# Optimization experiments

Measured on AMD Instinct MI355X. Metric: run time of the kernel, lower is better.

Reference implementation:

```python
import jax, jax.numpy as jnp
import numpy as np

EPS = 1e-5
NUM_GROUPS = 8

def group_norm(x, gamma, beta):
    B, C, D, H, W = x.shape
    g = NUM_GROUPS
    xg = x.reshape(B, g, C // g, D, H, W)
    mu = xg.mean(axis=(2, 3, 4, 5), keepdims=True)
    var = xg.var(axis=(2, 3, 4, 5), keepdims=True)
    xn = ((xg - mu) / jnp.sqrt(var + EPS)).reshape(B, C, D, H, W)
    return xn * gamma[None, :, None, None, None] + beta[None, :, None, None, None]

def setup_inputs() -> dict:
    key = jax.random.key(0)
    ks = jax.random.split(key, 7)
    B, C, D, H, W = 4, 256, 16, 16, 16
    x = jax.random.normal(ks[0], (B, C, D, H, W), dtype=jnp.float32)
    gn_gamma = jnp.ones((C,), dtype=jnp.float32)
    gn_beta = jnp.zeros((C,), dtype=jnp.float32)
    # 1x1x1 conv weights stored as [out, in] matrices
    s = 1.0 / np.sqrt(C)
    qkv_w = jax.random.uniform(ks[1], (3 * C, C), minval=-s, maxval=s, dtype=jnp.float32)
    qkv_b = jax.random.uniform(ks[2], (3 * C,), minval=-s, maxval=s, dtype=jnp.float32)
    proj_w = jax.random.uniform(ks[3], (C, C), minval=-s, maxval=s, dtype=jnp.float32)
    proj_b = jax.random.uniform(ks[4], (C,), minval=-s, maxval=s, dtype=jnp.float32)
    return {"x": x, "gn_gamma": gn_gamma, "gn_beta": gn_beta,
            "qkv_w": qkv_w, "qkv_b": qkv_b, "proj_w": proj_w, "proj_b": proj_b}

def reference(x, gn_gamma, gn_beta, qkv_w, qkv_b, proj_w, proj_b):
    B, C, D, H, W = x.shape
    N = D * H * W
    h = group_norm(x, gn_gamma, gn_beta)
    hf = h.reshape(B, C, N)  # (B, C, N)
    # 1x1x1 conv == channel matmul
    qkv = jnp.einsum('oc,bcn->bon', qkv_w, hf) + qkv_b[None, :, None]  # (B, 3C, N)
    q, k, v = jnp.split(qkv, 3, axis=1)  # each (B, C, N)
    q = q.transpose(0, 2, 1)  # (B, N, C)
    k = k.transpose(0, 2, 1)
    v = v.transpose(0, 2, 1)
    scale = C ** (-0.5)
    attn = jnp.einsum('bnc,bmc->bnm', q, k) * scale  # (B, N, N)
    attn = jax.nn.softmax(attn, axis=-1)
    o = jnp.einsum('bnm,bmc->bnc', attn, v)  # (B, N, C)
    o = o.transpose(0, 2, 1)  # (B, C, N)
    o = jnp.einsum('oc,bcn->bon', proj_w, o) + proj_b[None, :, None]
    return x + o.reshape(B, C, D, H, W)
```

## Files before the change

kernel.cpp:

```cpp
#include <hip/hip_runtime.h>
#include <hip/hip_bf16.h>

typedef unsigned short u16;
typedef unsigned int u32;
typedef __attribute__((ext_vector_type(8))) short short8;
typedef __attribute__((ext_vector_type(4))) short short4v;
typedef __attribute__((ext_vector_type(4))) float f32x4;

static __device__ __forceinline__ u16 f2bf(float f) {
    union { float f; unsigned u; } a; a.f = f;
    unsigned u = a.u;
    u += 0x7FFFu + ((u >> 16) & 1u);
    return (u16)(u >> 16);
}
static __device__ __forceinline__ float bf2f(u16 h) {
    union { u32 u; float f; } a; a.u = ((u32)h) << 16; return a.f;
}
static __device__ __forceinline__ u32 cvtpk(float lo, float hi) {
    u32 r; asm("v_cvt_pk_bf16_f32 %0, %1, %2" : "=v"(r) : "v"(lo), "v"(hi)); return r;
}
static __device__ __forceinline__ void gload16(const u16* g, u16* l) {
    __builtin_amdgcn_global_load_lds((const __attribute__((address_space(1))) u32*)(const void*)g,
                                     (__attribute__((address_space(3))) u32*)(void*)l, 16, 0, 0);
}

__global__ __launch_bounds__(256) void k_pre(const float* __restrict__ x, float* __restrict__ pstats,
                                             const float* __restrict__ qw, const float* __restrict__ pw,
                                             u16* __restrict__ q2, u16* __restrict__ p2) {
    const int t = threadIdx.x;
    if (blockIdx.x >= 256) {
        const int i = ((int)blockIdx.x - 256) * 1024 + t * 4;
        const float* src; u16* dst;
        if (i < 196608) { src = qw + i; dst = q2 + i; }
        else            { src = pw + (i - 196608); dst = p2 + (i - 196608); }
        float4 v = *reinterpret_cast<const float4*>(src);
        u16 o[4] = { f2bf(v.x), f2bf(v.y), f2bf(v.z), f2bf(v.w) };
        *reinterpret_cast<uint2*>(dst) = *reinterpret_cast<uint2*>(o);
        return;
    }
    const int bg = blockIdx.x >> 3, sl = blockIdx.x & 7;
    const float* p = x + (size_t)bg * 131072 + sl * 16384;
    float s = 0.f, ss = 0.f;
#pragma unroll
    for (int i = t * 4; i < 16384; i += 256 * 4) {
        float4 v = *reinterpret_cast<const float4*>(p + i);
        s  += v.x + v.y + v.z + v.w;
        ss += v.x * v.x + v.y * v.y + v.z * v.z + v.w * v.w;
    }
    for (int off = 1; off < 64; off <<= 1) { s += __shfl_xor(s, off); ss += __shfl_xor(ss, off); }
    __shared__ float ls[4], lss[4];
    if ((t & 63) == 0) { ls[t >> 6] = s; lss[t >> 6] = ss; }
    __syncthreads();
    if (t == 0) {
        pstats[(bg * 8 + sl) * 2]     = ls[0] + ls[1] + ls[2] + ls[3];
        pstats[(bg * 8 + sl) * 2 + 1] = lss[0] + lss[1] + lss[2] + lss[3];
    }
}

__global__ __launch_bounds__(256) void k_norm(const float* __restrict__ x, const float* __restrict__ gamma,
                                              const float* __restrict__ beta, const float* __restrict__ pstats,
                                              u16* __restrict__ H) {
    __shared__ u16 T[64][72];
    __shared__ float smu[2], srs[2];
    const int b = blockIdx.z, c0 = blockIdx.y * 64, n0 = blockIdx.x * 64;
    const int t = threadIdx.x;
    if (t < 2) {
        const int g = (c0 >> 5) + t;
        float S = 0.f, SS = 0.f;
#pragma unroll
        for (int sl = 0; sl < 8; ++sl) {
            S  += pstats[((b * 8 + g) * 8 + sl) * 2];
            SS += pstats[((b * 8 + g) * 8 + sl) * 2 + 1];
        }
        const float inv = 1.f / (32.f * 4096.f);
        float mu  = S * inv;
        float var = SS * inv - mu * mu;
        smu[t] = mu;
        srs[t] = rsqrtf(var + 1e-5f);
    }
    __syncthreads();
    const int cl = t >> 2, nb = (t & 3) * 16;
    const int c = c0 + cl;
    const float mu = smu[cl >> 5];
    const float rstd = srs[cl >> 5];
    const float ga = gamma[c] * rstd, be = beta[c] - mu * ga;
    const float* xp = &x[((size_t)b * 256 + c) * 4096 + n0 + nb];
#pragma unroll
    for (int j = 0; j < 16; j += 4) {
        float4 v = *reinterpret_cast<const float4*>(xp + j);
        T[cl][nb + j + 0] = f2bf(v.x * ga + be);
        T[cl][nb + j + 1] = f2bf(v.y * ga + be);
        T[cl][nb + j + 2] = f2bf(v.z * ga + be);
        T[cl][nb + j + 3] = f2bf(v.w * ga + be);
    }
    __syncthreads();
    const int nl = t >> 2, cb = (t & 3) * 16;
    short8 s0, s1;
#pragma unroll
    for (int j = 0; j < 8; ++j) { s0[j] = (short)T[cb + j][nl]; s1[j] = (short)T[cb + 8 + j][nl]; }
    u16* dst = &H[((size_t)b * 4096 + n0 + nl) * 256 + c0 + cb];
    *reinterpret_cast<short8*>(dst)     = s0;
    *reinterpret_cast<short8*>(dst + 8) = s1;
}

__global__ __launch_bounds__(256) void k_qkv(const u16* __restrict__ H, const u16* __restrict__ W2,
                                             const float* __restrict__ qkv_b,
                                             u16* __restrict__ Q, u16* __restrict__ K, u16* __restrict__ V) {
    __shared__ u16 T[9216];
    const int b = blockIdx.z, o0 = blockIdx.x * 64, nb0 = blockIdx.y * 128;
    const int t = threadIdx.x, w = t >> 6, l = t & 63, lr = l & 15, lg = l >> 4;
    const size_t bN = (size_t)b * 4096;
    f32x4 acc[2][4];
#pragma unroll
    for (int m = 0; m < 2; ++m)
#pragma unroll
        for (int nf = 0; nf < 4; ++nf) acc[m][nf] = f32x4{0.f, 0.f, 0.f, 0.f};
    const u16* A0 = &H[(bN + nb0 + w * 32 + lr) * 256];
    const u16* A1 = A0 + 16 * 256;
#pragma unroll
    for (int cc = 0; cc < 8; ++cc) {
        short8 af0 = *reinterpret_cast<const short8*>(A0 + cc * 32 + lg * 8);
        short8 af1 = *reinterpret_cast<const short8*>(A1 + cc * 32 + lg * 8);
#pragma unroll
        for (int nf = 0; nf < 4; ++nf) {
            short8 bf = *reinterpret_cast<const short8*>(&W2[(size_t)(o0 + nf * 16 + lr) * 256 + cc * 32 + lg * 8]);
            acc[0][nf] = __builtin_amdgcn_mfma_f32_16x16x32_bf16(af0, bf, acc[0][nf], 0, 0, 0);
            acc[1][nf] = __builtin_amdgcn_mfma_f32_16x16x32_bf16(af1, bf, acc[1][nf], 0, 0, 0);
        }
    }
    const int og = o0 >> 8;
    const float scal = (og == 0) ? 0.0625f * 1.44269504f : 1.0f;
    float bias[4];
#pragma unroll
    for (int nf = 0; nf < 4; ++nf) bias[nf] = qkv_b[o0 + nf * 16 + lr];
    if (og < 2) {
#pragma unroll
        for (int m = 0; m < 2; ++m)
#pragma unroll
            for (int nf = 0; nf < 4; ++nf)
#pragma unroll
                for (int i = 0; i < 4; ++i)
                    T[(w * 32 + m * 16 + lg * 4 + i) * 72 + nf * 16 + lr] = f2bf((acc[m][nf][i] + bias[nf]) * scal);
        __syncthreads();
        const int rl = t >> 1, half = (t & 1) * 32;
        u16* dst = (og == 0 ? Q : K) + (bN + nb0 + rl) * 256 + (o0 & 255) + half;
#pragma unroll
        for (int j = 0; j < 4; ++j)
            *reinterpret_cast<short8*>(dst + j * 8) = *reinterpret_cast<short8*>(&T[rl * 72 + half + j * 8]);
    } else {
#pragma unroll
        for (int m = 0; m < 2; ++m)
#pragma unroll
            for (int nf = 0; nf < 4; ++nf)
#pragma unroll
                for (int i = 0; i < 4; ++i)
                    T[(nf * 16 + lr) * 144 + w * 32 + m * 16 + lg * 4 + i] = f2bf(acc[m][nf][i] + bias[nf]);
        __syncthreads();
        const int ol = t >> 2, nbl = (t & 3) * 32;
        const int s_ = (ol >> 1) & 7;
        u16* dst = V + ((size_t)b * 256 + (o0 - 512) + ol) * 4096 + nb0 + nbl;
#pragma unroll
        for (int j = 0; j < 4; ++j) {
            short8 vv = *reinterpret_cast<short8*>(&T[ol * 144 + nbl + j * 8]);
            short8 ov;
            if (s_ & 1) ov = short8{vv[4], vv[5], vv[6], vv[7], vv[0], vv[1], vv[2], vv[3]};
            else        ov = vv;
            *reinterpret_cast<short8*>(dst + (((2 * j) ^ (s_ & 6)) * 4)) = ov;
        }
    }
}

__global__ __launch_bounds__(512, 1) void k_flash(const u16* __restrict__ Qw, const u16* __restrict__ Kw,
                                                  const u16* __restrict__ Vw, u16* __restrict__ Opart,
                                                  float* __restrict__ ml) {
    __shared__ u16 Ks[2][16384];
    __shared__ u16 Vs[2][16384];
    const int sp = blockIdx.x, b = blockIdx.y;
    const int tid = threadIdx.x;
    const int w = tid >> 6, l = tid & 63;
    const int lr = l & 15, lg = l >> 4;
    const int qbase = blockIdx.z * 256 + w * 32;
    const int kb0 = sp * 1024;
    const size_t bN = (size_t)b * 4096;

    const u16* srcK = Kw + (bN + kb0 + (tid >> 5)) * 256 + (((tid & 31) * 8) ^ (((tid >> 5) & 7) * 8));
    const int u = tid & 255, sth = tid >> 8;
    const u16* srcV = Vw + ((size_t)b * 256 + (u >> 2)) * 4096 + kb0 + sth * 32 + (u & 3) * 8;
    const int vdst = sth * 8192 + u * 8;

#define STAGE(d, toff) { \
        const u16* sk_ = srcK + (size_t)(toff) * 16384; \
        const u16* sv_ = srcV + (toff) * 64; \
        gload16(sk_,               Ks[d] + tid * 8); \
        gload16(sk_ + 16 * 256,    Ks[d] + 4096 + tid * 8); \
        gload16(sk_ + 32 * 256,    Ks[d] + 8192 + tid * 8); \
        gload16(sk_ + 48 * 256,    Ks[d] + 12288 + tid * 8); \
        gload16(sv_,               Vs[d] + vdst); \
        gload16(sv_ + 64 * 4096,   Vs[d] + vdst + 2048); \
        gload16(sv_ + 128 * 4096,  Vs[d] + vdst + 4096); \
        gload16(sv_ + 192 * 4096,  Vs[d] + vdst + 6144); }

    const int c6 = (lr >> 2) & 1;
    int kofs[2];
#pragma unroll
    for (int n = 0; n < 2; ++n) kofs[n] = (n * 16 + lr) * 256 + ((lg * 8) ^ ((lr & 3) * 8));
    const int vslotA = ((lg ^ (lr >> 1)) * 4);
    const int vslotB = vslotA ^ 16;

    short8 qf[2][8];
#pragma unroll
    for (int m = 0; m < 2; ++m)
#pragma unroll
        for (int cc = 0; cc < 8; ++cc)
            qf[m][cc] = *reinterpret_cast<const short8*>(&Qw[(bN + qbase + m * 16 + lr) * 256 + cc * 32 + lg * 8]);

    f32x4 Oa[2][16];
    float mr[2], lsum[2];
#pragma unroll
    for (int m = 0; m < 2; ++m) {
#pragma unroll
        for (int cs = 0; cs < 16; ++cs) Oa[m][cs] = f32x4{0.f, 0.f, 0.f, 0.f};
        mr[m] = -1e30f; lsum[m] = 0.f;
    }

#define QK_PHASE(scv, ST) { \
        const int kO_ = (ST) * 8192; \
        _Pragma("unroll") \
        for (int m = 0; m < 2; ++m) \
            _Pragma("unroll") \
            for (int n = 0; n < 2; ++n) scv[m][n] = f32x4{0.f, 0.f, 0.f, 0.f}; \
        __builtin_amdgcn_s_setprio(1); \
        _Pragma("unroll") \
        for (int cc = 0; cc < 8; ++cc) { \
            const int cb_ = ((cc ^ c6) << 5); \
            short8 kf0 = *reinterpret_cast<const short8*>(&Ks[d][kO_ + kofs[0] + cb_]); \
            short8 kf1 = *reinterpret_cast<const short8*>(&Ks[d][kO_ + kofs[1] + cb_]); \
            scv[0][0] = __builtin_amdgcn_mfma_f32_16x16x32_bf16(kf0, qf[0][cc], scv[0][0], 0, 0, 0); \
            scv[0][1] = __builtin_amdgcn_mfma_f32_16x16x32_bf16(kf1, qf[0][cc], scv[0][1], 0, 0, 0); \
            scv[1][0] = __builtin_amdgcn_mfma_f32_16x16x32_bf16(kf0, qf[1][cc], scv[1][0], 0, 0, 0); \
            scv[1][1] = __builtin_amdgcn_mfma_f32_16x16x32_bf16(kf1, qf[1][cc], scv[1][1], 0, 0, 0); \
        } \
        __builtin_amdgcn_s_setprio(0); }

#define SM_PHASE(scv, pfv) { \
        float tmax_[2]; \
        bool need_ = false; \
        _Pragma("unroll") \
        for (int m = 0; m < 2; ++m) { \
            float tm = fmaxf(fmaxf(fmaxf(scv[m][0][0], scv[m][0][1]), fmaxf(scv[m][0][2], scv[m][0][3])), \
                             fmaxf(fmaxf(scv[m][1][0], scv[m][1][1]), fmaxf(scv[m][1][2], scv[m][1][3]))); \
            tm = fmaxf(tm, __shfl_xor(tm, 16)); \
            tm = fmaxf(tm, __shfl_xor(tm, 32)); \
            tmax_[m] = tm; \
            need_ = need_ || (tm > mr[m] + 8.f); \
        } \
        if (__any(need_)) { \
            float av_[2][4]; \
            _Pragma("unroll") \
            for (int m = 0; m < 2; ++m) { \
                float mn = fmaxf(mr[m], tmax_[m]); \
                float al = exp2f(mr[m] - mn); \
                mr[m] = mn; \
                lsum[m] *= al; \
                _Pragma("unroll") \
                for (int i = 0; i < 4; ++i) av_[m][i] = __shfl(al, lg * 4 + i); \
            } \
            _Pragma("unroll") \
            for (int m = 0; m < 2; ++m) \
                _Pragma("unroll") \
                for (int cs = 0; cs < 16; ++cs) \
                    _Pragma("unroll") \
                    for (int i = 0; i < 4; ++i) Oa[m][cs][i] *= av_[m][i]; \
        } \
        _Pragma("unroll") \
        for (int m = 0; m < 2; ++m) { \
            float p_[8]; \
            float la_ = 0.f; \
            _Pragma("unroll") \
            for (int n = 0; n < 2; ++n) \
                _Pragma("unroll") \
                for (int i = 0; i < 4; ++i) { \
                    float pv = exp2f(scv[m][n][i] - mr[m]); \
                    la_ += pv; \
                    p_[n * 4 + i] = pv; \
                } \
            lsum[m] += la_; \
            _Pragma("unroll") \
            for (int j = 0; j < 4; ++j) pfv[m][j] = cvtpk(p_[2 * j], p_[2 * j + 1]); \
        } }

#define PV_PHASE(pfv, ST) { \
        const int vH_ = (ST) * 8192; \
        union { u32 uw[4]; short8 v; } pa_, pb_; \
        _Pragma("unroll") \
        for (int j = 0; j < 4; ++j) { pa_.uw[j] = pfv[0][j]; pb_.uw[j] = pfv[1][j]; } \
        __builtin_amdgcn_s_setprio(1); \
        _Pragma("unroll") \
        for (int cs = 0; cs < 16; ++cs) { \
            const int base_ = vH_ + (cs * 16 + lr) * 32; \
            short4v lo = *reinterpret_cast<const short4v*>(&Vs[d][base_ + vslotA]); \
            short4v hi = *reinterpret_cast<const short4v*>(&Vs[d][base_ + vslotB]); \
            short8 vf = __builtin_shufflevector(lo, hi, 0, 1, 2, 3, 4, 5, 6, 7); \
            Oa[0][cs] = __builtin_amdgcn_mfma_f32_16x16x32_bf16(pa_.v, vf, Oa[0][cs], 0, 0, 0); \
            Oa[1][cs] = __builtin_amdgcn_mfma_f32_16x16x32_bf16(pb_.v, vf, Oa[1][cs], 0, 0, 0); \
        } \
        __builtin_amdgcn_s_setprio(0); }

    STAGE(0, 0);
    for (int kt = 0; kt < 16; ++kt) {
        const int d = kt & 1;
        asm volatile("s_waitcnt vmcnt(0)" ::: "memory");
        __builtin_amdgcn_sched_barrier(0);
        __builtin_amdgcn_s_barrier();
        if (kt < 15) STAGE(d ^ 1, kt + 1);

        f32x4 sc[2][2];
        u32 pf0[2][4], pf1[2][4];
        QK_PHASE(sc, 0);
        SM_PHASE(sc, pf0);
        QK_PHASE(sc, 1);
        PV_PHASE(pf0, 0);
        SM_PHASE(sc, pf1);
        PV_PHASE(pf1, 1);
    }
#undef STAGE
#undef QK_PHASE
#undef SM_PHASE
#undef PV_PHASE

    float lt[2];
#pragma unroll
    for (int m = 0; m < 2; ++m) {
        float ts = lsum[m];
        ts += __shfl_xor(ts, 16);
        ts += __shfl_xor(ts, 32);
        lt[m] = ts;
    }
    const size_t obase = ((size_t)(b * 4 + sp) * 4096 + qbase);
#pragma unroll
    for (int m = 0; m < 2; ++m)
#pragma unroll
        for (int cs = 0; cs < 16; ++cs)
#pragma unroll
            for (int i = 0; i < 4; ++i)
                Opart[(obase + m * 16 + lg * 4 + i) * 256 + cs * 16 + lr] = f2bf(Oa[m][cs][i]);
    if (lg == 0) {
#pragma unroll
        for (int m = 0; m < 2; ++m) {
            size_t r = obase + m * 16 + lr;
            ml[r * 2]     = mr[m];
            ml[r * 2 + 1] = lt[m];
        }
    }
}

__global__ __launch_bounds__(256) void k_comb(const u16* __restrict__ Opart, const float* __restrict__ ml,
                                              u16* __restrict__ Obf) {
    const int row = blockIdx.x * 8 + (threadIdx.x >> 5);
    const int b = row >> 12;
    const int c0 = (threadIdx.x & 31) * 8;
    const size_t rbase = (size_t)b * 4 * 4096 + (row & 4095);
    float ms[4], lsv[4];
#pragma unroll
    for (int s = 0; s < 4; ++s) {
        ms[s]  = ml[(rbase + (size_t)s * 4096) * 2];
        lsv[s] = ml[(rbase + (size_t)s * 4096) * 2 + 1];
    }
    float M = fmaxf(fmaxf(ms[0], ms[1]), fmaxf(ms[2], ms[3]));
    float W[4], L = 0.f;
#pragma unroll
    for (int s = 0; s < 4; ++s) { W[s] = exp2f(ms[s] - M); L += W[s] * lsv[s]; }
    const float inv = 1.f / L;
    float o[8] = {};
#pragma unroll
    for (int s = 0; s < 4; ++s) {
        short8 v = *reinterpret_cast<const short8*>(&Opart[(rbase + (size_t)s * 4096) * 256 + c0]);
#pragma unroll
        for (int j = 0; j < 8; ++j) o[j] += W[s] * bf2f((u16)v[j]);
    }
    short8 r;
#pragma unroll
    for (int j = 0; j < 8; ++j) r[j] = (short)f2bf(o[j] * inv);
    *reinterpret_cast<short8*>(&Obf[(size_t)row * 256 + c0]) = r;
}

__global__ __launch_bounds__(256) void k_proj(const u16* __restrict__ O, const u16* __restrict__ Wp,
                                              const float* __restrict__ proj_b, const float* __restrict__ x,
                                              float* __restrict__ out) {
    __shared__ float T[64][132];
    const int b = blockIdx.z, c0 = blockIdx.x * 64, nb0 = blockIdx.y * 128;
    const int t = threadIdx.x, w = t >> 6, l = t & 63, lr = l & 15, lg = l >> 4;
    const size_t bN = (size_t)b * 4096;
    f32x4 acc[2][4];
#pragma unroll
    for (int m = 0; m < 2; ++m)
#pragma unroll
        for (int nf = 0; nf < 4; ++nf) acc[m][nf] = f32x4{0.f, 0.f, 0.f, 0.f};
    const u16* A0 = &O[(bN + nb0 + w * 32 + lr) * 256];
    const u16* A1 = A0 + 16 * 256;
#pragma unroll
    for (int cc = 0; cc < 8; ++cc) {
        short8 af0 = *reinterpret_cast<const short8*>(A0 + cc * 32 + lg * 8);
        short8 af1 = *reinterpret_cast<const short8*>(A1 + cc * 32 + lg * 8);
#pragma unroll
        for (int nf = 0; nf < 4; ++nf) {
            short8 bf = *reinterpret_cast<const short8*>(&Wp[(size_t)(c0 + nf * 16 + lr) * 256 + cc * 32 + lg * 8]);
            acc[0][nf] = __builtin_amdgcn_mfma_f32_16x16x32_bf16(af0, bf, acc[0][nf], 0, 0, 0);
            acc[1][nf] = __builtin_amdgcn_mfma_f32_16x16x32_bf16(af1, bf, acc[1][nf], 0, 0, 0);
        }
    }
#pragma unroll
    for (int m = 0; m < 2; ++m)
#pragma unroll
        for (int nf = 0; nf < 4; ++nf)
#pragma unroll
            for (int i = 0; i < 4; ++i)
                T[nf * 16 + lr][w * 32 + m * 16 + lg * 4 + i] = acc[m][nf][i];
    __syncthreads();
    const int cl = t >> 2, nbl = (t & 3) * 32;
    const float pb = proj_b[c0 + cl];
    const size_t base = ((size_t)b * 256 + c0 + cl) * 4096 + nb0 + nbl;
#pragma unroll
    for (int j = 0; j < 32; j += 4) {
        float4 xv = *reinterpret_cast<const float4*>(&x[base + j]);
        float4 r;
        r.x = xv.x + T[cl][nbl + j + 0] + pb;
        r.y = xv.y + T[cl][nbl + j + 1] + pb;
        r.z = xv.z + T[cl][nbl + j + 2] + pb;
        r.w = xv.w + T[cl][nbl + j + 3] + pb;
        *reinterpret_cast<float4*>(&out[base + j]) = r;
    }
}

extern "C" void kernel_launch(void* const* d_in, const int* in_sizes, int n_in,
                              void* d_out, int out_size, void* d_ws, size_t ws_size,
                              hipStream_t stream) {
    const float* x      = (const float*)d_in[0];
    const float* gngam  = (const float*)d_in[1];
    const float* gnbeta = (const float*)d_in[2];
    const float* qkv_w  = (const float*)d_in[3];
    const float* qkv_b  = (const float*)d_in[4];
    const float* proj_w = (const float*)d_in[5];
    const float* proj_b = (const float*)d_in[6];
    float* out = (float*)d_out;

    char* wsb = (char*)d_ws;
    float* pstats = (float*)wsb;
    u16* Hbf   = (u16*)(wsb + 4096);
    u16* Qws   = Hbf + 4194304;
    u16* Kws   = Qws + 4194304;
    u16* Vws   = Kws + 4194304;
    u16* W2q   = Vws + 4194304;
    u16* W2p   = W2q + 196608;
    u16* Opart = W2p + 65536;
    float* ml  = (float*)(Opart + 16777216);
    u16* Obf   = (u16*)(ml + 131072);

    k_pre<<<512, 256, 0, stream>>>(x, pstats, qkv_w, proj_w, W2q, W2p);
    k_norm<<<dim3(64, 4, 4), 256, 0, stream>>>(x, gngam, gnbeta, pstats, Hbf);
    k_qkv<<<dim3(12, 32, 4), 256, 0, stream>>>(Hbf, W2q, qkv_b, Qws, Kws, Vws);
    k_flash<<<dim3(4, 4, 16), 512, 0, stream>>>(Qws, Kws, Vws, Opart, ml);
    k_comb<<<2048, 256, 0, stream>>>(Opart, ml, Obf);
    k_proj<<<dim3(4, 32, 4), 256, 0, stream>>>(Obf, W2p, proj_b, x, out);
}
```

Baseline: 164.9 us.

## Fuse split-KV combine into flash kernel via last-block atomic counter

Removes the separate k_comb launch. Each flash block now increments a per-(batch, query-tile) counter after writing its partial output, and the last of the four split blocks merges the partials into Obf. This saves a kernel launch and its gap, but adds a memset launch and makes the combine serial in one block per tile, which can leave a tail where few blocks are still active.

```diff
diff --git a/kernel.cpp b/kernel.cpp
--- a/kernel.cpp
+++ b/kernel.cpp
@@ -172,7 +172,8 @@
 
 __global__ __launch_bounds__(512, 1) void k_flash(const u16* __restrict__ Qw, const u16* __restrict__ Kw,
                                                   const u16* __restrict__ Vw, u16* __restrict__ Opart,
-                                                  float* __restrict__ ml) {
+                                                  float* __restrict__ ml, u16* __restrict__ Obf,
+                                                  int* __restrict__ cnt) {
     __shared__ u16 Ks[2][16384];
     __shared__ u16 Vs[2][16384];
     const int sp = blockIdx.x, b = blockIdx.y;
@@ -352,36 +353,44 @@
             ml[r * 2 + 1] = lt[m];
         }
     }
-}
-
-__global__ __launch_bounds__(256) void k_comb(const u16* __restrict__ Opart, const float* __restrict__ ml,
-                                              u16* __restrict__ Obf) {
-    const int row = blockIdx.x * 8 + (threadIdx.x >> 5);
-    const int b = row >> 12;
-    const int c0 = (threadIdx.x & 31) * 8;
-    const size_t rbase = (size_t)b * 4 * 4096 + (row & 4095);
-    float ms[4], lsv[4];
-#pragma unroll
-    for (int s = 0; s < 4; ++s) {
-        ms[s]  = ml[(rbase + (size_t)s * 4096) * 2];
-        lsv[s] = ml[(rbase + (size_t)s * 4096) * 2 + 1];
-    }
-    float M = fmaxf(fmaxf(ms[0], ms[1]), fmaxf(ms[2], ms[3]));
-    float W[4], L = 0.f;
-#pragma unroll
-    for (int s = 0; s < 4; ++s) { W[s] = exp2f(ms[s] - M); L += W[s] * lsv[s]; }
-    const float inv = 1.f / L;
-    float o[8] = {};
-#pragma unroll
-    for (int s = 0; s < 4; ++s) {
-        short8 v = *reinterpret_cast<const short8*>(&Opart[(rbase + (size_t)s * 4096) * 256 + c0]);
-#pragma unroll
-        for (int j = 0; j < 8; ++j) o[j] += W[s] * bf2f((u16)v[j]);
-    }
-    short8 r;
-#pragma unroll
-    for (int j = 0; j < 8; ++j) r[j] = (short)f2bf(o[j] * inv);
-    *reinterpret_cast<short8*>(&Obf[(size_t)row * 256 + c0]) = r;
+
+    __threadfence();
+    __syncthreads();
+    __shared__ int lastFlag;
+    if (tid == 0) lastFlag = (atomicAdd(&cnt[b * 16 + blockIdx.z], 1) == 3);
+    __syncthreads();
+    if (lastFlag) {
+        __threadfence();
+        const int qt0 = blockIdx.z * 256;
+        const size_t base0 = (size_t)(b * 4) * 4096;
+        for (int it = tid; it < 8192; it += 512) {
+            const int rr = it >> 5;
+            const int c0 = (it & 31) * 8;
+            const size_t rbase = base0 + qt0 + rr;
+            float ms[4], lsv[4];
+#pragma unroll
+            for (int s = 0; s < 4; ++s) {
+                ms[s]  = ml[(rbase + (size_t)s * 4096) * 2];
+                lsv[s] = ml[(rbase + (size_t)s * 4096) * 2 + 1];
+            }
+            float M = fmaxf(fmaxf(ms[0], ms[1]), fmaxf(ms[2], ms[3]));
+            float W[4], L = 0.f;
+#pragma unroll
+            for (int s = 0; s < 4; ++s) { W[s] = exp2f(ms[s] - M); L += W[s] * lsv[s]; }
+            const float inv = 1.f / L;
+            float o[8] = {};
+#pragma unroll
+            for (int s = 0; s < 4; ++s) {
+                short8 v = *reinterpret_cast<const short8*>(&Opart[(rbase + (size_t)s * 4096) * 256 + c0]);
+#pragma unroll
+                for (int j = 0; j < 8; ++j) o[j] += W[s] * bf2f((u16)v[j]);
+            }
+            short8 r;
+#pragma unroll
+            for (int j = 0; j < 8; ++j) r[j] = (short)f2bf(o[j] * inv);
+            *reinterpret_cast<short8*>(&Obf[((size_t)b * 4096 + qt0 + rr) * 256 + c0]) = r;
+        }
+    }
 }
 
 __global__ __launch_bounds__(256) void k_proj(const u16* __restrict__ O, const u16* __restrict__ Wp,
@@ -454,12 +463,13 @@
     u16* W2p   = W2q + 196608;
     u16* Opart = W2p + 65536;
     float* ml  = (float*)(Opart + 16777216);
-    u16* Obf   = (u16*)(ml + 131072);
-
+    int* cnt   = (int*)(ml + 131072);
+    u16* Obf   = (u16*)(cnt + 64);
+
+    hipMemsetAsync(cnt, 0, 64 * sizeof(int), stream);
     k_pre<<<512, 256, 0, stream>>>(x, pstats, qkv_w, proj_w, W2q, W2p);
     k_norm<<<dim3(64, 4, 4), 256, 0, stream>>>(x, gngam, gnbeta, pstats, Hbf);
     k_qkv<<<dim3(12, 32, 4), 256, 0, stream>>>(Hbf, W2q, qkv_b, Qws, Kws, Vws);
-    k_flash<<<dim3(4, 4, 16), 512, 0, stream>>>(Qws, Kws, Vws, Opart, ml);
-    k_comb<<<2048, 256, 0, stream>>>(Opart, ml, Obf);
+    k_flash<<<dim3(4, 4, 16), 512, 0, stream>>>(Qws, Kws, Vws, Opart, ml, Obf, cnt);
     k_proj<<<dim3(4, 32, 4), 256, 0, stream>>>(Obf, W2p, proj_b, x, out);
 }
```

Result: slower. 271.7 us (+64.8%).
